# Kernel tuning notes

Hardware: AMD Instinct MI355X
Metric: run time of the kernel (lower is better)

Reference implementation:

```python
import jax, jax.numpy as jnp
import numpy as np

H = W = 128
SCALE = 4
Q = (SCALE * H) * (SCALE * W)
C = 64
E = 4


def _conv2d(x, w, b, pad):
    y = jax.lax.conv_general_dilated(x, w, (1, 1), [(pad, pad), (pad, pad)],
                                     dimension_numbers=('NCHW', 'OIHW', 'NCHW'))
    return y + b[None, :, None, None]


def _conv1x1(x, w, b):
    return jnp.einsum('oc,bchw->bohw', w, x) + b[None, :, None, None]


def _bilinear_zeros(img, gx, gy):
    # img: [C,Hs,Ws]; gx,gy: [Hh,Wh] normalized coords, align_corners=True, zeros padding
    c, Hs, Ws = img.shape
    x = (gx + 1.0) * 0.5 * (Ws - 1)
    y = (gy + 1.0) * 0.5 * (Hs - 1)
    x0 = jnp.floor(x)
    y0 = jnp.floor(y)
    wx1 = x - x0; wx0 = 1.0 - wx1
    wy1 = y - y0; wy0 = 1.0 - wy1
    x0i = x0.astype(jnp.int32); y0i = y0.astype(jnp.int32)

    def gather(yi, xi):
        m = ((xi >= 0) & (xi < Ws) & (yi >= 0) & (yi < Hs)).astype(img.dtype)
        v = img[:, jnp.clip(yi, 0, Hs - 1), jnp.clip(xi, 0, Ws - 1)]
        return v * m  # [C,Hh,Wh]

    return (gather(y0i, x0i) * (wy0 * wx0) + gather(y0i, x0i + 1) * (wy0 * wx1)
            + gather(y0i + 1, x0i) * (wy1 * wx0) + gather(y0i + 1, x0i + 1) * (wy1 * wx1))


def setup_inputs() -> dict:
    key = jax.random.key(0)
    ks = jax.random.split(key, 18)
    s = 0.1
    d = {}
    d['inp'] = jax.random.normal(ks[0], (1, 3, H, W), jnp.float32)
    d['coord'] = jax.random.uniform(ks[1], (1, Q, 2), jnp.float32, -1.0, 1.0)
    d['cell'] = jnp.full((1, Q, 2), 2.0 / (SCALE * H), jnp.float32)  # cell = 2/(scale*h) exactly
    d['enc_w'] = jax.random.normal(ks[2], (C, 3, 3, 3), jnp.float32) * s
    d['enc_b'] = jax.random.normal(ks[3], (C,), jnp.float32) * s
    d['body_w1'] = jax.random.normal(ks[4], (C, 4), jnp.float32) * s
    d['body_b1'] = jax.random.normal(ks[5], (C,), jnp.float32) * s
    d['body_w2'] = jax.random.normal(ks[6], (C, C), jnp.float32) * s
    d['body_b2'] = jax.random.normal(ks[7], (C,), jnp.float32) * s
    d['routing_w'] = jax.random.normal(ks[8], (E, C), jnp.float32) * s
    d['routing_b'] = jax.random.normal(ks[9], (E,), jnp.float32) * s
    d['offset_w'] = jax.random.normal(ks[10], (2, C), jnp.float32) * s
    d['offset_b'] = jax.random.normal(ks[11], (2,), jnp.float32) * s
    d['tail_w'] = jax.random.normal(ks[12], (3, C, 3, 3), jnp.float32) * s
    d['tail_b'] = jax.random.normal(ks[13], (3,), jnp.float32) * s
    d['weight_compress'] = jax.random.normal(ks[14], (E, C // 8, C), jnp.float32) * s
    d['weight_expand'] = jax.random.normal(ks[15], (E, C, C // 8), jnp.float32) * s
    d['scale'] = SCALE
    return d


def reference(inp, coord, cell, enc_w, enc_b, body_w1, body_b1, body_w2, body_b2,
              routing_w, routing_b, offset_w, offset_b, tail_w, tail_b,
              weight_compress, weight_expand, scale):
    feat = _conv2d(inp, enc_w, enc_b, pad=1)        # encoder -> [1,64,h,w]
    _, c, h, w = feat.shape
    Hh, Wh = scale * h, scale * w
    fs = float(scale)

    # scale embedding input: [1/scale, 1/scale, coor_h, coor_w]
    ih = jnp.arange(Hh, dtype=jnp.float32)
    iw = jnp.arange(Wh, dtype=jnp.float32)
    coor_h = (ih + 0.5) / fs - jnp.floor((ih + 0.5) / fs + 0.001) - 0.5
    coor_w = (iw + 0.5) / fs - jnp.floor((iw + 0.5) / fs + 0.001) - 0.5
    cs = jnp.full((Hh, Wh), 1.0 / fs, jnp.float32)
    inp4 = jnp.stack([cs, cs,
                      jnp.broadcast_to(coor_h[:, None], (Hh, Wh)),
                      jnp.broadcast_to(coor_w[None, :], (Hh, Wh))])[None]  # [1,4,Hh,Wh]

    emb = jax.nn.relu(_conv1x1(inp4, body_w1, body_b1))
    emb = jax.nn.relu(_conv1x1(emb, body_w2, body_b2))
    off = _conv1x1(emb, offset_w, offset_b)[0]                 # [2,Hh,Wh]
    r = jax.nn.sigmoid(_conv1x1(emb, routing_w, routing_b))[0]  # [E,Hh,Wh]

    # offset grid_sample of LR feat onto HR grid (align_corners=True, zeros pad)
    xx, yy = jnp.meshgrid(jnp.arange(Wh, dtype=jnp.float32), jnp.arange(Hh, dtype=jnp.float32))
    gx = (((xx + 0.5) / fs - 0.5) * 2.0 / (w - 1) - 1.0) + off[0] * 2.0 / (w - 1)
    gy = (((yy + 0.5) / fs - 0.5) * 2.0 / (h - 1) - 1.0) + off[1] * 2.0 / (h - 1)
    fea0 = _bilinear_zeros(feat[0], gx, gy)                    # [c,Hh,Wh]

    # per-pixel expert mixing; linear in routing, so apply experts then mix
    t = jnp.einsum('ekc,chw->ekhw', weight_compress, fea0)     # [E,c/8,Hh,Wh]
    mid = jnp.einsum('ehw,ekhw->khw', r, t)                    # [c/8,Hh,Wh]
    u = jnp.einsum('eck,khw->echw', weight_expand, mid)        # [E,c,Hh,Wh]
    out2 = jnp.einsum('ehw,echw->chw', r, u)                   # [c,Hh,Wh]

    pred = _conv2d((out2 + fea0)[None], tail_w, tail_b, pad=1)[0]  # [3,Hh,Wh]

    # nearest-neighbour query (align_corners=True)
    coord_q = jnp.clip(coord - cell * 0.5 + 1e-6, -1.0 + 1e-6, 1.0 - 1e-6)[0]  # [Q,2] (y,x)
    gxq = coord_q[:, 1]
    gyq = coord_q[:, 0]
    xi = jnp.clip(jnp.round((gxq + 1.0) * 0.5 * (Wh - 1)).astype(jnp.int32), 0, Wh - 1)
    yi = jnp.clip(jnp.round((gyq + 1.0) * 0.5 * (Hh - 1)).astype(jnp.int32), 0, Hh - 1)
    q = pred[:, yi, xi].T                                      # [Q,3]
    return q[None]                                             # [1,Q,3]
```

## Files before the change

kernel.cpp:

```cpp
#include <hip/hip_runtime.h>
#include <hip/hip_bf16.h>

typedef __hip_bfloat16 bf16;
typedef __fp16 h2 __attribute__((ext_vector_type(2)));

__device__ __forceinline__ float bf2f(bf16 h) { return __bfloat162float(h); }
__device__ __forceinline__ bf16 us2bf(unsigned short u){ union{unsigned short s; bf16 h;}v; v.s=u; return v.h; }
__device__ __forceinline__ float asf(unsigned u){ union{unsigned u; float f;}v; v.u=u; return v.f; }
__device__ __forceinline__ h2 uh(unsigned u){ union{unsigned u; h2 h;}v; v.u=u; return v.h; }
__device__ __forceinline__ unsigned pkh(float a, float b){ union{h2 h; unsigned u;}v; v.h=__builtin_amdgcn_cvt_pkrtz(a,b); return v.u; }
__device__ __forceinline__ unsigned short f2bu(float a){ union{bf16 h; unsigned short u;}v; v.h=__float2bfloat16(a); return v.u; }
__device__ __forceinline__ unsigned pkbf(float a, float b){ return ((unsigned)f2bu(b) << 16) | (unsigned)f2bu(a); }
#define FDOT2(va,vb,acc) __builtin_amdgcn_fdot2((va),(vb),(acc),false)

#define HH 128
#define WW 128
#define HS 512
#define WSZ 512
#define QN (HS*WSZ)

#define O_OFFTAB 0
#define O_TB     32
#define O_TW2    64
#define O_CWC2   1024
#define O_W2P    5120
#define O_FEAT   8192
#define O_PRED   1056768

#define SH_W2T 0
#define SH_WE  4160
#define SH_WC  6208
#define SH_TW  8256
#define SH_OW  9984
#define SH_RW  10112
#define SH_END 10368

__constant__ int PREF2[16] = {0,15,27,39,54,64,72,80,90,100,108,116,126,141,153,165};

__device__ __forceinline__ float rdin(const void* p, int i, bool f32m) {
  return f32m ? ((const float*)p)[i] : bf2f(((const bf16*)p)[i]);
}
__device__ __forceinline__ float rdw(const void* p, int i, bool f32m) {
  if (f32m) return ((const float*)p)[i];
  unsigned u = ((const unsigned*)p)[i>>1];
  return asf((i&1) ? (u & 0xffff0000u) : (u<<16));
}
__device__ __forceinline__ bool sniff_f32(const void* inp) {
  int lane = threadIdx.x & 63;
  unsigned short u = ((const unsigned short*)inp)[2*lane];
  float v = bf2f(us2bf(u));
  bool ok = (v == v) && (fabsf(v) < 64.0f);
  return __popcll(__ballot(ok)) < 48;
}
__device__ __forceinline__ unsigned blend4(unsigned a, unsigned b, unsigned c, unsigned d,
                                           h2 W00, h2 W01, h2 W10, h2 W11) {
  h2 f = uh(a)*W00 + uh(b)*W01 + uh(c)*W10 + uh(d)*W11;
  union{h2 h; unsigned u;} v; v.h = f; return v.u;
}

__global__ __launch_bounds__(256) void k_prep(
    const void* __restrict__ inp, const void* __restrict__ encw, const void* __restrict__ encb,
    const void* __restrict__ w1, const void* __restrict__ b1,
    const void* __restrict__ w2, const void* __restrict__ b2,
    const void* __restrict__ rw, const void* __restrict__ rb,
    const void* __restrict__ ow, const void* __restrict__ ob,
    const void* __restrict__ tw, const void* __restrict__ tb,
    const void* __restrict__ wc, const void* __restrict__ we,
    float* __restrict__ ws) {
  __shared__ float shpool[SH_END];
  __shared__ float sh1[64];
  __shared__ float sh2[64];
  __shared__ float shr[4];
  __shared__ float shcwe[512];
  bool f32m = sniff_f32(inp);
  int b = blockIdx.x, t = threadIdx.x;
  unsigned* wsu = (unsigned*)ws;

  if (b < 256) {
    int g = b >> 6;
    int px = (b & 63)*256 + t;
    float* shw = shpool;
    float* shb = shpool + 432;
    for (int i = t; i < 432; i += 256) shw[i] = rdw(encw, g*432 + i, f32m);
    if (t < 16) shb[t] = rdw(encb, g*16 + t, f32m);
    __syncthreads();
    int x = px & 127, y = px >> 7;
    float tp[27];
    #pragma unroll
    for (int ic = 0; ic < 3; ic++)
      #pragma unroll
      for (int dy = 0; dy < 3; dy++) {
        int yy = y + dy - 1;
        #pragma unroll
        for (int dx = 0; dx < 3; dx++) {
          int xx = x + dx - 1;
          bool ok = (yy >= 0) & (yy < 128) & (xx >= 0) & (xx < 128);
          tp[ic*9 + dy*3 + dx] = ok ? rdin(inp, ic*16384 + yy*128 + xx, f32m) : 0.0f;
        }
      }
    unsigned e[8];
    #pragma unroll
    for (int o4 = 0; o4 < 4; o4++) {
      float a[4];
      #pragma unroll
      for (int oo = 0; oo < 4; oo++) {
        int o2 = o4*4 + oo;
        float acc = shb[o2];
        #pragma unroll
        for (int kk = 0; kk < 27; kk++) acc = fmaf(shw[o2*27 + kk], tp[kk], acc);
        a[oo] = acc;
      }
      e[o4*2]   = pkh(a[0], a[1]);
      e[o4*2+1] = pkh(a[2], a[3]);
    }
    uint4* outp = (uint4*)(wsu + O_FEAT + px*32 + g*8);
    outp[0] = make_uint4(e[0], e[1], e[2], e[3]);
    outp[1] = make_uint4(e[4], e[5], e[6], e[7]);
  } else if (b < 272) {
    int cls = b - 256;
    for (int i = t; i < 4096; i += 256) shpool[SH_W2T + (i & 63)*65 + (i >> 6)] = rdw(w2, i, f32m);
    for (int i = t; i < 2048; i += 256) { shpool[SH_WE + i] = rdw(we, i, f32m); shpool[SH_WC + i] = rdw(wc, i, f32m); }
    for (int i = t; i < 1728; i += 256) shpool[SH_TW + i] = rdw(tw, i, f32m);
    for (int i = t; i < 128; i += 256)  shpool[SH_OW + i] = rdw(ow, i, f32m);
    for (int i = t; i < 256; i += 256)  shpool[SH_RW + i] = rdw(rw, i, f32m);
    if (t < 64) {
      float mcls = (float)(cls >> 2), ncls = (float)(cls & 3);
      float chv = (mcls + 0.5f)*0.25f - 0.5f;
      float cwv = (ncls + 0.5f)*0.25f - 0.5f;
      float s1 = rdw(w1,t*4+0,f32m)*0.25f + rdw(w1,t*4+1,f32m)*0.25f
               + rdw(w1,t*4+2,f32m)*chv + rdw(w1,t*4+3,f32m)*cwv + rdw(b1,t,f32m);
      sh1[t] = fmaxf(s1, 0.0f);
    }
    __syncthreads();
    if (t < 64) {
      float s2 = rdw(b2,t,f32m);
      for (int i = 0; i < 64; i++) s2 = fmaf(shpool[SH_W2T + i*65 + t], sh1[i], s2);
      sh2[t] = fmaxf(s2, 0.0f);
    }
    __syncthreads();
    if (t < 2) {
      float a = rdw(ob,t,f32m);
      for (int i = 0; i < 64; i++) a = fmaf(shpool[SH_OW + t*64 + i], sh2[i], a);
      ws[O_OFFTAB + cls*2 + t] = a;
    } else if (t < 6) {
      int e = t - 2;
      float a = rdw(rb,e,f32m);
      for (int i = 0; i < 64; i++) a = fmaf(shpool[SH_RW + e*64 + i], sh2[i], a);
      shr[e] = 1.0f / (1.0f + expf(-a));
    }
    __syncthreads();
    float r0 = shr[0], r1 = shr[1], r2 = shr[2], r3 = shr[3];
    for (int idx = t; idx < 512; idx += 256) {
      float a =       r0 * shpool[SH_WE + idx];
      a = fmaf(r1, shpool[SH_WE +  512 + idx], a);
      a = fmaf(r2, shpool[SH_WE + 1024 + idx], a);
      a = fmaf(r3, shpool[SH_WE + 1536 + idx], a);
      shcwe[idx] = a;
    }
    unsigned* wcw = wsu + O_CWC2 + cls*256;
    for (int idx = t; idx < 256; idx += 256) {
      int cp = idx >> 3, k = idx & 7;
      float lo =       r0 * shpool[SH_WC +        k*64 + 2*cp];
      lo = fmaf(r1, shpool[SH_WC +  512 + k*64 + 2*cp], lo);
      lo = fmaf(r2, shpool[SH_WC + 1024 + k*64 + 2*cp], lo);
      lo = fmaf(r3, shpool[SH_WC + 1536 + k*64 + 2*cp], lo);
      float hi =       r0 * shpool[SH_WC +        k*64 + 2*cp + 1];
      hi = fmaf(r1, shpool[SH_WC +  512 + k*64 + 2*cp + 1], hi);
      hi = fmaf(r2, shpool[SH_WC + 1024 + k*64 + 2*cp + 1], hi);
      hi = fmaf(r3, shpool[SH_WC + 1536 + k*64 + 2*cp + 1], hi);
      wcw[idx] = pkh(lo, hi);
    }
    __syncthreads();
    unsigned* wpp = wsu + O_W2P;
    for (int idx = t; idx < 108; idx += 256) {
      int j = idx / 12, rem = idx - j*12, o2 = rem >> 2, kp = rem & 3;
      float alo = 0.0f, ahi = 0.0f;
      for (int c = 0; c < 64; c++) {
        float tv = shpool[SH_TW + (o2*64 + c)*9 + j];
        alo = fmaf(tv, shcwe[c*8 + 2*kp],     alo);
        ahi = fmaf(tv, shcwe[c*8 + 2*kp + 1], ahi);
      }
      wpp[(cls*9 + j)*12 + o2*4 + kp] = pkh(alo, ahi);
    }
  } else {
    for (int idx = t; idx < 864; idx += 256) {
      int o2 = idx / 288, rem = idx - o2*288, j = rem >> 5, cp = rem & 31;
      unsigned d = pkh(rdw(tw, (o2*64 + 2*cp    )*9 + j, f32m),
                       rdw(tw, (o2*64 + 2*cp + 1)*9 + j, f32m));
      (wsu + O_TW2)[idx] = d;
    }
    if (t < 3) ws[O_TB + t] = rdin(tb, t, f32m);
  }
}

__global__ __launch_bounds__(256) void k_maintail(const float* __restrict__ ws, unsigned* __restrict__ pred4) {
  __shared__ unsigned shf[32*181];
  __shared__ __align__(16) unsigned shm4[181*4];
  __shared__ unsigned short sof[192];
  __shared__ unsigned short scls[192];
  __shared__ float spart[128*3];
  const unsigned* wsu = (const unsigned*)ws;
  int blk = blockIdx.x;
  int xcd = blk & 7, local = blk >> 3;
  int ty0 = (xcd*8 + (local >> 5)) * 8;
  int tx0 = (local & 31) * 16;
  int t = threadIdx.x;
  int q = t & 1;
  const uint4* F2 = (const uint4*)(wsu + O_FEAT);

  for (int s0 = 0; s0 < 256; s0 += 128) {
    int s = s0 + (t >> 1);
    if (s >= 180) continue;
    int cls = 0;
    #pragma unroll
    for (int i = 1; i < 16; i++) cls += (s >= PREF2[i]) ? 1 : 0;
    int j = s - PREF2[cls];
    int a = cls >> 2, bb = cls & 3;
    int nx = ((bb == 0) | (bb == 3)) ? 5 : 4;
    int jy = (nx == 4) ? (j >> 2) : ((j*13) >> 6);
    int jx = j - jy*nx;
    int py = ((a + 1) & 3) + 4*jy;
    int px = ((bb + 1) & 3) + 4*jx;
    int pos = py*18 + px;
    if (q == 0) sof[pos] = (unsigned short)s;
    int gy = ty0 - 1 + py, gx = tx0 - 1 + px;
    if ((gy < 0) | (gy >= HS) | (gx < 0) | (gx >= WSZ)) {
      if (q == 0) scls[s] = 0;
      #pragma unroll
      for (int i = 0; i < 16; i++) shf[(q*16 + i)*181 + s] = 0u;
      shm4[s*4 + q*2 + 0] = 0u;
      shm4[s*4 + q*2 + 1] = 0u;
      continue;
    }
    if (q == 0) scls[s] = (unsigned short)cls;
    float off0 = ws[O_OFFTAB + cls*2 + 0];
    float off1 = ws[O_OFFTAB + cls*2 + 1];
    float gxf = (((float)gx + 0.5f)*0.25f - 0.5f)*(2.0f/127.0f) - 1.0f + off0*(2.0f/127.0f);
    float gyf = (((float)gy + 0.5f)*0.25f - 0.5f)*(2.0f/127.0f) - 1.0f + off1*(2.0f/127.0f);
    float sx = (gxf + 1.0f)*0.5f*127.0f;
    float sy = (gyf + 1.0f)*0.5f*127.0f;
    float x0f = floorf(sx), y0f = floorf(sy);
    float fx = sx - x0f, fy = sy - y0f;
    int ix0 = (int)x0f, iy0 = (int)y0f;
    int ix1 = ix0 + 1, iy1 = iy0 + 1;
    float wx0 = 1.0f - fx, wy0 = 1.0f - fy;
    float w00 = wy0*wx0, w01 = wy0*fx, w10 = fy*wx0, w11 = fy*fx;
    bool vx0 = (ix0 >= 0) & (ix0 < WW), vx1 = (ix1 >= 0) & (ix1 < WW);
    bool vy0 = (iy0 >= 0) & (iy0 < HH), vy1 = (iy1 >= 0) & (iy1 < HH);
    if (!(vy0 & vx0)) w00 = 0.0f;
    if (!(vy0 & vx1)) w01 = 0.0f;
    if (!(vy1 & vx0)) w10 = 0.0f;
    if (!(vy1 & vx1)) w11 = 0.0f;
    int cx0 = min(max(ix0, 0), WW-1), cx1 = min(max(ix1, 0), WW-1);
    int cy0 = min(max(iy0, 0), HH-1), cy1 = min(max(iy1, 0), HH-1);
    int b00 = (cy0*WW + cx0)*8 + q*4, b01 = (cy0*WW + cx1)*8 + q*4;
    int b10 = (cy1*WW + cx0)*8 + q*4, b11 = (cy1*WW + cx1)*8 + q*4;

    uint4 A0 = F2[b00+0], A1 = F2[b00+1], A2 = F2[b00+2], A3 = F2[b00+3];
    uint4 B0 = F2[b01+0], B1 = F2[b01+1], B2 = F2[b01+2], B3 = F2[b01+3];
    uint4 C0 = F2[b10+0], C1 = F2[b10+1], C2 = F2[b10+2], C3 = F2[b10+3];
    uint4 D0 = F2[b11+0], D1 = F2[b11+1], D2 = F2[b11+2], D3 = F2[b11+3];

    h2 W00 = { (__fp16)w00, (__fp16)w00 };
    h2 W01 = { (__fp16)w01, (__fp16)w01 };
    h2 W10 = { (__fp16)w10, (__fp16)w10 };
    h2 W11 = { (__fp16)w11, (__fp16)w11 };

    unsigned fp[16];
    fp[ 0] = blend4(A0.x,B0.x,C0.x,D0.x,W00,W01,W10,W11);
    fp[ 1] = blend4(A0.y,B0.y,C0.y,D0.y,W00,W01,W10,W11);
    fp[ 2] = blend4(A0.z,B0.z,C0.z,D0.z,W00,W01,W10,W11);
    fp[ 3] = blend4(A0.w,B0.w,C0.w,D0.w,W00,W01,W10,W11);
    fp[ 4] = blend4(A1.x,B1.x,C1.x,D1.x,W00,W01,W10,W11);
    fp[ 5] = blend4(A1.y,B1.y,C1.y,D1.y,W00,W01,W10,W11);
    fp[ 6] = blend4(A1.z,B1.z,C1.z,D1.z,W00,W01,W10,W11);
    fp[ 7] = blend4(A1.w,B1.w,C1.w,D1.w,W00,W01,W10,W11);
    fp[ 8] = blend4(A2.x,B2.x,C2.x,D2.x,W00,W01,W10,W11);
    fp[ 9] = blend4(A2.y,B2.y,C2.y,D2.y,W00,W01,W10,W11);
    fp[10] = blend4(A2.z,B2.z,C2.z,D2.z,W00,W01,W10,W11);
    fp[11] = blend4(A2.w,B2.w,C2.w,D2.w,W00,W01,W10,W11);
    fp[12] = blend4(A3.x,B3.x,C3.x,D3.x,W00,W01,W10,W11);
    fp[13] = blend4(A3.y,B3.y,C3.y,D3.y,W00,W01,W10,W11);
    fp[14] = blend4(A3.z,B3.z,C3.z,D3.z,W00,W01,W10,W11);
    fp[15] = blend4(A3.w,B3.w,C3.w,D3.w,W00,W01,W10,W11);

    #pragma unroll
    for (int i = 0; i < 16; i++) shf[(q*16 + i)*181 + s] = fp[i];

    const uint4* CWv = (const uint4*)(wsu + O_CWC2 + cls*256) + q*32;
    float mid[8] = {0,0,0,0,0,0,0,0};
    #pragma unroll
    for (int i = 0; i < 16; i++) {
      uint4 w0 = CWv[i*2], w1 = CWv[i*2+1];
      h2 f = uh(fp[i]);
      mid[0] = FDOT2(f, uh(w0.x), mid[0]); mid[1] = FDOT2(f, uh(w0.y), mid[1]);
      mid[2] = FDOT2(f, uh(w0.z), mid[2]); mid[3] = FDOT2(f, uh(w0.w), mid[3]);
      mid[4] = FDOT2(f, uh(w1.x), mid[4]); mid[5] = FDOT2(f, uh(w1.y), mid[5]);
      mid[6] = FDOT2(f, uh(w1.z), mid[6]); mid[7] = FDOT2(f, uh(w1.w), mid[7]);
    }
    #pragma unroll
    for (int k = 0; k < 8; k++) mid[k] += __shfl_xor(mid[k], 1);
    shm4[s*4 + q*2 + 0] = pkh(mid[q*4+0], mid[q*4+1]);
    shm4[s*4 + q*2 + 1] = pkh(mid[q*4+2], mid[q*4+3]);
  }
  __syncthreads();

  int half = t >> 7, pi = t & 127;
  int tx = pi & 15, ty = pi >> 4;
  int slots[9];
  #pragma unroll
  for (int dy = 0; dy < 3; dy++)
    #pragma unroll
    for (int dx = 0; dx < 3; dx++)
      slots[dy*3 + dx] = sof[(ty + dy)*18 + (tx + dx)];
  const unsigned* TW2 = wsu + O_TW2;
  float a0, a1, a2;
  if (half == 0) { a0 = ws[O_TB+0]; a1 = ws[O_TB+1]; a2 = ws[O_TB+2]; }
  else           { a0 = 0.0f; a1 = 0.0f; a2 = 0.0f; }
  int cp0 = half*16;
  for (int cpl = 0; cpl < 16; cpl++) {
    int cp = cp0 + cpl;
    #pragma unroll
    for (int j = 0; j < 9; j++) {
      h2 hv = uh(shf[cp*181 + slots[j]]);
      a0 = FDOT2(hv, uh(TW2[(0*9 + j)*32 + cp]), a0);
      a1 = FDOT2(hv, uh(TW2[(1*9 + j)*32 + cp]), a1);
      a2 = FDOT2(hv, uh(TW2[(2*9 + j)*32 + cp]), a2);
    }
  }
  {
    int jb = (half == 0) ? 0 : 5;
    int je = (half == 0) ? 5 : 9;
    for (int j = jb; j < je; j++) {
      int sl = slots[j];
      int cl = scls[sl];
      uint4 mv = *(const uint4*)&shm4[sl*4];
      const uint4* Wp = (const uint4*)(wsu + O_W2P) + (cl*9 + j)*3;
      uint4 w0 = Wp[0], w1 = Wp[1], w2 = Wp[2];
      h2 m0 = uh(mv.x), m1 = uh(mv.y), m2 = uh(mv.z), m3 = uh(mv.w);
      a0 = FDOT2(m0, uh(w0.x), a0); a0 = FDOT2(m1, uh(w0.y), a0);
      a0 = FDOT2(m2, uh(w0.z), a0); a0 = FDOT2(m3, uh(w0.w), a0);
      a1 = FDOT2(m0, uh(w1.x), a1); a1 = FDOT2(m1, uh(w1.y), a1);
      a1 = FDOT2(m2, uh(w1.z), a1); a1 = FDOT2(m3, uh(w1.w), a1);
      a2 = FDOT2(m0, uh(w2.x), a2); a2 = FDOT2(m1, uh(w2.y), a2);
      a2 = FDOT2(m2, uh(w2.z), a2); a2 = FDOT2(m3, uh(w2.w), a2);
    }
  }
  if (half == 1) {
    spart[pi*3+0] = a0; spart[pi*3+1] = a1; spart[pi*3+2] = a2;
  }
  __syncthreads();
  if (half == 0) {
    a0 += spart[pi*3+0]; a1 += spart[pi*3+1]; a2 += spart[pi*3+2];
    ((uint2*)pred4)[blk*128 + pi] = make_uint2(pkbf(a0, a1), pkbf(a2, 0.0f));
  }
}

__global__ __launch_bounds__(256) void k_gather(const void* __restrict__ inp,
                                                const void* __restrict__ coord, const void* __restrict__ cell,
                                                const float* __restrict__ ws, void* __restrict__ outp) {
  bool f32m = sniff_f32(inp);
  const uint2* pred4 = (const uint2*)((const unsigned*)ws + O_PRED);
  int q = blockIdx.x*256 + threadIdx.x;
  float cy, cx, ly, lx;
  if (f32m) {
    float2 c = ((const float2*)coord)[q]; cy = c.x; cx = c.y;
    float2 l = ((const float2*)cell)[q];  ly = l.x; lx = l.y;
  } else {
    unsigned cu = ((const unsigned*)coord)[q]; cy = asf(cu<<16); cx = asf(cu & 0xffff0000u);
    unsigned lu = ((const unsigned*)cell)[q];  ly = asf(lu<<16); lx = asf(lu & 0xffff0000u);
  }
  float gyq = fminf(fmaxf(cy - ly*0.5f + 1e-6f, -1.0f + 1e-6f), 1.0f - 1e-6f);
  float gxq = fminf(fmaxf(cx - lx*0.5f + 1e-6f, -1.0f + 1e-6f), 1.0f - 1e-6f);
  int xi = (int)rintf((gxq + 1.0f)*0.5f*511.0f);
  int yi = (int)rintf((gyq + 1.0f)*0.5f*511.0f);
  xi = min(max(xi, 0), WSZ-1);
  yi = min(max(yi, 0), HS-1);
  int row = yi >> 3, col = xi >> 4;
  int xcd = row >> 3;
  int local = (row & 7)*32 + col;
  int blk = local*8 + xcd;
  int pi = (yi & 7)*16 + (xi & 15);
  uint2 d = pred4[blk*128 + pi];
  float v0 = asf(d.x << 16), v1 = asf(d.x & 0xffff0000u), v2 = asf(d.y << 16);
  if (f32m) {
    float* o = (float*)outp;
    o[q*3 + 0] = v0; o[q*3 + 1] = v1; o[q*3 + 2] = v2;
  } else {
    bf16* o = (bf16*)outp;
    o[q*3 + 0] = __float2bfloat16(v0);
    o[q*3 + 1] = __float2bfloat16(v1);
    o[q*3 + 2] = __float2bfloat16(v2);
  }
}

extern "C" void kernel_launch(void* const* d_in, const int* in_sizes, int n_in,
                              void* d_out, int out_size, void* d_ws, size_t ws_size,
                              hipStream_t stream) {
  const void* inp   = d_in[0];
  const void* coord = d_in[1];
  const void* cell  = d_in[2];
  const void* encw  = d_in[3];
  const void* encb  = d_in[4];
  const void* w1    = d_in[5];
  const void* b1    = d_in[6];
  const void* w2    = d_in[7];
  const void* b2    = d_in[8];
  const void* rw    = d_in[9];
  const void* rb    = d_in[10];
  const void* ow    = d_in[11];
  const void* ob    = d_in[12];
  const void* tw    = d_in[13];
  const void* tb    = d_in[14];
  const void* wc    = d_in[15];
  const void* we    = d_in[16];

  float* wsf = (float*)d_ws;
  unsigned* pred4 = (unsigned*)wsf + O_PRED;

  k_prep<<<273, 256, 0, stream>>>(inp, encw, encb, w1, b1, w2, b2, rw, rb, ow, ob, tw, tb, wc, we, wsf);
  k_maintail<<<2048, 256, 0, stream>>>(wsf, pred4);
  k_gather<<<1024, 256, 0, stream>>>(inp, coord, cell, wsf, d_out);
}
```

Before: 176.8 us.

## Double block size in main tail kernel, split conv into four partial sums

```diff
diff --git a/kernel.cpp b/kernel.cpp
--- a/kernel.cpp
+++ b/kernel.cpp
@@ -193,12 +193,11 @@
   }
 }
 
-__global__ __launch_bounds__(256) void k_maintail(const float* __restrict__ ws, unsigned* __restrict__ pred4) {
+__global__ __launch_bounds__(512) void k_maintail(const float* __restrict__ ws, unsigned* __restrict__ pred4) {
   __shared__ unsigned shf[32*181];
   __shared__ __align__(16) unsigned shm4[181*4];
-  __shared__ unsigned short sof[192];
   __shared__ unsigned short scls[192];
-  __shared__ float spart[128*3];
+  __shared__ float spart[3*384];
   const unsigned* wsu = (const unsigned*)ws;
   int blk = blockIdx.x;
   int xcd = blk & 7, local = blk >> 3;
@@ -208,9 +207,8 @@
   int q = t & 1;
   const uint4* F2 = (const uint4*)(wsu + O_FEAT);
 
-  for (int s0 = 0; s0 < 256; s0 += 128) {
-    int s = s0 + (t >> 1);
-    if (s >= 180) continue;
+  int s = t >> 1;
+  if (s < 180) {
     int cls = 0;
     #pragma unroll
     for (int i = 1; i < 16; i++) cls += (s >= PREF2[i]) ? 1 : 0;
@@ -222,119 +220,119 @@
     int py = ((a + 1) & 3) + 4*jy;
     int px = ((bb + 1) & 3) + 4*jx;
     int pos = py*18 + px;
-    if (q == 0) sof[pos] = (unsigned short)s;
     int gy = ty0 - 1 + py, gx = tx0 - 1 + px;
     if ((gy < 0) | (gy >= HS) | (gx < 0) | (gx >= WSZ)) {
-      if (q == 0) scls[s] = 0;
-      #pragma unroll
-      for (int i = 0; i < 16; i++) shf[(q*16 + i)*181 + s] = 0u;
-      shm4[s*4 + q*2 + 0] = 0u;
-      shm4[s*4 + q*2 + 1] = 0u;
-      continue;
-    }
-    if (q == 0) scls[s] = (unsigned short)cls;
-    float off0 = ws[O_OFFTAB + cls*2 + 0];
-    float off1 = ws[O_OFFTAB + cls*2 + 1];
-    float gxf = (((float)gx + 0.5f)*0.25f - 0.5f)*(2.0f/127.0f) - 1.0f + off0*(2.0f/127.0f);
-    float gyf = (((float)gy + 0.5f)*0.25f - 0.5f)*(2.0f/127.0f) - 1.0f + off1*(2.0f/127.0f);
-    float sx = (gxf + 1.0f)*0.5f*127.0f;
-    float sy = (gyf + 1.0f)*0.5f*127.0f;
-    float x0f = floorf(sx), y0f = floorf(sy);
-    float fx = sx - x0f, fy = sy - y0f;
-    int ix0 = (int)x0f, iy0 = (int)y0f;
-    int ix1 = ix0 + 1, iy1 = iy0 + 1;
-    float wx0 = 1.0f - fx, wy0 = 1.0f - fy;
-    float w00 = wy0*wx0, w01 = wy0*fx, w10 = fy*wx0, w11 = fy*fx;
-    bool vx0 = (ix0 >= 0) & (ix0 < WW), vx1 = (ix1 >= 0) & (ix1 < WW);
-    bool vy0 = (iy0 >= 0) & (iy0 < HH), vy1 = (iy1 >= 0) & (iy1 < HH);
-    if (!(vy0 & vx0)) w00 = 0.0f;
-    if (!(vy0 & vx1)) w01 = 0.0f;
-    if (!(vy1 & vx0)) w10 = 0.0f;
-    if (!(vy1 & vx1)) w11 = 0.0f;
-    int cx0 = min(max(ix0, 0), WW-1), cx1 = min(max(ix1, 0), WW-1);
-    int cy0 = min(max(iy0, 0), HH-1), cy1 = min(max(iy1, 0), HH-1);
-    int b00 = (cy0*WW + cx0)*8 + q*4, b01 = (cy0*WW + cx1)*8 + q*4;
-    int b10 = (cy1*WW + cx0)*8 + q*4, b11 = (cy1*WW + cx1)*8 + q*4;
-
-    uint4 A0 = F2[b00+0], A1 = F2[b00+1], A2 = F2[b00+2], A3 = F2[b00+3];
-    uint4 B0 = F2[b01+0], B1 = F2[b01+1], B2 = F2[b01+2], B3 = F2[b01+3];
-    uint4 C0 = F2[b10+0], C1 = F2[b10+1], C2 = F2[b10+2], C3 = F2[b10+3];
-    uint4 D0 = F2[b11+0], D1 = F2[b11+1], D2 = F2[b11+2], D3 = F2[b11+3];
-
-    h2 W00 = { (__fp16)w00, (__fp16)w00 };
-    h2 W01 = { (__fp16)w01, (__fp16)w01 };
-    h2 W10 = { (__fp16)w10, (__fp16)w10 };
-    h2 W11 = { (__fp16)w11, (__fp16)w11 };
-
-    unsigned fp[16];
-    fp[ 0] = blend4(A0.x,B0.x,C0.x,D0.x,W00,W01,W10,W11);
-    fp[ 1] = blend4(A0.y,B0.y,C0.y,D0.y,W00,W01,W10,W11);
-    fp[ 2] = blend4(A0.z,B0.z,C0.z,D0.z,W00,W01,W10,W11);
-    fp[ 3] = blend4(A0.w,B0.w,C0.w,D0.w,W00,W01,W10,W11);
-    fp[ 4] = blend4(A1.x,B1.x,C1.x,D1.x,W00,W01,W10,W11);
-    fp[ 5] = blend4(A1.y,B1.y,C1.y,D1.y,W00,W01,W10,W11);
-    fp[ 6] = blend4(A1.z,B1.z,C1.z,D1.z,W00,W01,W10,W11);
-    fp[ 7] = blend4(A1.w,B1.w,C1.w,D1.w,W00,W01,W10,W11);
-    fp[ 8] = blend4(A2.x,B2.x,C2.x,D2.x,W00,W01,W10,W11);
-    fp[ 9] = blend4(A2.y,B2.y,C2.y,D2.y,W00,W01,W10,W11);
-    fp[10] = blend4(A2.z,B2.z,C2.z,D2.z,W00,W01,W10,W11);
-    fp[11] = blend4(A2.w,B2.w,C2.w,D2.w,W00,W01,W10,W11);
-    fp[12] = blend4(A3.x,B3.x,C3.x,D3.x,W00,W01,W10,W11);
-    fp[13] = blend4(A3.y,B3.y,C3.y,D3.y,W00,W01,W10,W11);
-    fp[14] = blend4(A3.z,B3.z,C3.z,D3.z,W00,W01,W10,W11);
-    fp[15] = blend4(A3.w,B3.w,C3.w,D3.w,W00,W01,W10,W11);
-
-    #pragma unroll
-    for (int i = 0; i < 16; i++) shf[(q*16 + i)*181 + s] = fp[i];
-
-    const uint4* CWv = (const uint4*)(wsu + O_CWC2 + cls*256) + q*32;
-    float mid[8] = {0,0,0,0,0,0,0,0};
-    #pragma unroll
-    for (int i = 0; i < 16; i++) {
-      uint4 w0 = CWv[i*2], w1 = CWv[i*2+1];
-      h2 f = uh(fp[i]);
-      mid[0] = FDOT2(f, uh(w0.x), mid[0]); mid[1] = FDOT2(f, uh(w0.y), mid[1]);
-      mid[2] = FDOT2(f, uh(w0.z), mid[2]); mid[3] = FDOT2(f, uh(w0.w), mid[3]);
-      mid[4] = FDOT2(f, uh(w1.x), mid[4]); mid[5] = FDOT2(f, uh(w1.y), mid[5]);
-      mid[6] = FDOT2(f, uh(w1.z), mid[6]); mid[7] = FDOT2(f, uh(w1.w), mid[7]);
-    }
-    #pragma unroll
-    for (int k = 0; k < 8; k++) mid[k] += __shfl_xor(mid[k], 1);
-    shm4[s*4 + q*2 + 0] = pkh(mid[q*4+0], mid[q*4+1]);
-    shm4[s*4 + q*2 + 1] = pkh(mid[q*4+2], mid[q*4+3]);
+      if (q == 0) scls[pos] = 0;
+      #pragma unroll
+      for (int i = 0; i < 16; i++) shf[(q*16 + i)*181 + pos] = 0u;
+      shm4[pos*4 + q*2 + 0] = 0u;
+      shm4[pos*4 + q*2 + 1] = 0u;
+    } else {
+      if (q == 0) scls[pos] = (unsigned short)cls;
+      float off0 = ws[O_OFFTAB + cls*2 + 0];
+      float off1 = ws[O_OFFTAB + cls*2 + 1];
+      float gxf = (((float)gx + 0.5f)*0.25f - 0.5f)*(2.0f/127.0f) - 1.0f + off0*(2.0f/127.0f);
+      float gyf = (((float)gy + 0.5f)*0.25f - 0.5f)*(2.0f/127.0f) - 1.0f + off1*(2.0f/127.0f);
+      float sx = (gxf + 1.0f)*0.5f*127.0f;
+      float sy = (gyf + 1.0f)*0.5f*127.0f;
+      float x0f = floorf(sx), y0f = floorf(sy);
+      float fx = sx - x0f, fy = sy - y0f;
+      int ix0 = (int)x0f, iy0 = (int)y0f;
+      int ix1 = ix0 + 1, iy1 = iy0 + 1;
+      float wx0 = 1.0f - fx, wy0 = 1.0f - fy;
+      float w00 = wy0*wx0, w01 = wy0*fx, w10 = fy*wx0, w11 = fy*fx;
+      bool vx0 = (ix0 >= 0) & (ix0 < WW), vx1 = (ix1 >= 0) & (ix1 < WW);
+      bool vy0 = (iy0 >= 0) & (iy0 < HH), vy1 = (iy1 >= 0) & (iy1 < HH);
+      if (!(vy0 & vx0)) w00 = 0.0f;
+      if (!(vy0 & vx1)) w01 = 0.0f;
+      if (!(vy1 & vx0)) w10 = 0.0f;
+      if (!(vy1 & vx1)) w11 = 0.0f;
+      int cx0 = min(max(ix0, 0), WW-1), cx1 = min(max(ix1, 0), WW-1);
+      int cy0 = min(max(iy0, 0), HH-1), cy1 = min(max(iy1, 0), HH-1);
+      int b00 = (cy0*WW + cx0)*8 + q*4, b01 = (cy0*WW + cx1)*8 + q*4;
+      int b10 = (cy1*WW + cx0)*8 + q*4, b11 = (cy1*WW + cx1)*8 + q*4;
+
+      uint4 A0 = F2[b00+0], A1 = F2[b00+1], A2 = F2[b00+2], A3 = F2[b00+3];
+      uint4 B0 = F2[b01+0], B1 = F2[b01+1], B2 = F2[b01+2], B3 = F2[b01+3];
+      uint4 C0 = F2[b10+0], C1 = F2[b10+1], C2 = F2[b10+2], C3 = F2[b10+3];
+      uint4 D0 = F2[b11+0], D1 = F2[b11+1], D2 = F2[b11+2], D3 = F2[b11+3];
+
+      h2 W00 = { (__fp16)w00, (__fp16)w00 };
+      h2 W01 = { (__fp16)w01, (__fp16)w01 };
+      h2 W10 = { (__fp16)w10, (__fp16)w10 };
+      h2 W11 = { (__fp16)w11, (__fp16)w11 };
+
+      unsigned fp[16];
+      fp[ 0] = blend4(A0.x,B0.x,C0.x,D0.x,W00,W01,W10,W11);
+      fp[ 1] = blend4(A0.y,B0.y,C0.y,D0.y,W00,W01,W10,W11);
+      fp[ 2] = blend4(A0.z,B0.z,C0.z,D0.z,W00,W01,W10,W11);
+      fp[ 3] = blend4(A0.w,B0.w,C0.w,D0.w,W00,W01,W10,W11);
+      fp[ 4] = blend4(A1.x,B1.x,C1.x,D1.x,W00,W01,W10,W11);
+      fp[ 5] = blend4(A1.y,B1.y,C1.y,D1.y,W00,W01,W10,W11);
+      fp[ 6] = blend4(A1.z,B1.z,C1.z,D1.z,W00,W01,W10,W11);
+      fp[ 7] = blend4(A1.w,B1.w,C1.w,D1.w,W00,W01,W10,W11);
+      fp[ 8] = blend4(A2.x,B2.x,C2.x,D2.x,W00,W01,W10,W11);
+      fp[ 9] = blend4(A2.y,B2.y,C2.y,D2.y,W00,W01,W10,W11);
+      fp[10] = blend4(A2.z,B2.z,C2.z,D2.z,W00,W01,W10,W11);
+      fp[11] = blend4(A2.w,B2.w,C2.w,D2.w,W00,W01,W10,W11);
+      fp[12] = blend4(A3.x,B3.x,C3.x,D3.x,W00,W01,W10,W11);
+      fp[13] = blend4(A3.y,B3.y,C3.y,D3.y,W00,W01,W10,W11);
+      fp[14] = blend4(A3.z,B3.z,C3.z,D3.z,W00,W01,W10,W11);
+      fp[15] = blend4(A3.w,B3.w,C3.w,D3.w,W00,W01,W10,W11);
+
+      #pragma unroll
+      for (int i = 0; i < 16; i++) shf[(q*16 + i)*181 + pos] = fp[i];
+
+      const uint4* CWv = (const uint4*)(wsu + O_CWC2 + cls*256) + q*32;
+      float mid[8] = {0,0,0,0,0,0,0,0};
+      #pragma unroll
+      for (int i = 0; i < 16; i++) {
+        uint4 w0 = CWv[i*2], w1 = CWv[i*2+1];
+        h2 f = uh(fp[i]);
+        mid[0] = FDOT2(f, uh(w0.x), mid[0]); mid[1] = FDOT2(f, uh(w0.y), mid[1]);
+        mid[2] = FDOT2(f, uh(w0.z), mid[2]); mid[3] = FDOT2(f, uh(w0.w), mid[3]);
+        mid[4] = FDOT2(f, uh(w1.x), mid[4]); mid[5] = FDOT2(f, uh(w1.y), mid[5]);
+        mid[6] = FDOT2(f, uh(w1.z), mid[6]); mid[7] = FDOT2(f, uh(w1.w), mid[7]);
+      }
+      #pragma unroll
+      for (int k = 0; k < 8; k++) mid[k] += __shfl_xor(mid[k], 1);
+      shm4[pos*4 + q*2 + 0] = pkh(mid[q*4+0], mid[q*4+1]);
+      shm4[pos*4 + q*2 + 1] = pkh(mid[q*4+2], mid[q*4+3]);
+    }
   }
   __syncthreads();
 
-  int half = t >> 7, pi = t & 127;
+  int split = t >> 7, pi = t & 127;
   int tx = pi & 15, ty = pi >> 4;
-  int slots[9];
+  int pos9[9];
   #pragma unroll
   for (int dy = 0; dy < 3; dy++)
     #pragma unroll
     for (int dx = 0; dx < 3; dx++)
-      slots[dy*3 + dx] = sof[(ty + dy)*18 + (tx + dx)];
+      pos9[dy*3 + dx] = (ty + dy)*18 + (tx + dx);
   const unsigned* TW2 = wsu + O_TW2;
   float a0, a1, a2;
-  if (half == 0) { a0 = ws[O_TB+0]; a1 = ws[O_TB+1]; a2 = ws[O_TB+2]; }
-  else           { a0 = 0.0f; a1 = 0.0f; a2 = 0.0f; }
-  int cp0 = half*16;
-  for (int cpl = 0; cpl < 16; cpl++) {
+  if (split == 0) { a0 = ws[O_TB+0]; a1 = ws[O_TB+1]; a2 = ws[O_TB+2]; }
+  else            { a0 = 0.0f; a1 = 0.0f; a2 = 0.0f; }
+  int cp0 = split*8;
+  for (int cpl = 0; cpl < 8; cpl++) {
     int cp = cp0 + cpl;
     #pragma unroll
     for (int j = 0; j < 9; j++) {
-      h2 hv = uh(shf[cp*181 + slots[j]]);
+      h2 hv = uh(shf[cp*181 + pos9[j]]);
       a0 = FDOT2(hv, uh(TW2[(0*9 + j)*32 + cp]), a0);
       a1 = FDOT2(hv, uh(TW2[(1*9 + j)*32 + cp]), a1);
       a2 = FDOT2(hv, uh(TW2[(2*9 + j)*32 + cp]), a2);
     }
   }
   {
-    int jb = (half == 0) ? 0 : 5;
-    int je = (half == 0) ? 5 : 9;
+    const int JB[4] = {0, 2, 5, 7};
+    const int JE[4] = {2, 5, 7, 9};
+    int jb = JB[split], je = JE[split];
     for (int j = jb; j < je; j++) {
-      int sl = slots[j];
-      int cl = scls[sl];
-      uint4 mv = *(const uint4*)&shm4[sl*4];
+      int pp = pos9[j];
+      int cl = scls[pp];
+      uint4 mv = *(const uint4*)&shm4[pp*4];
       const uint4* Wp = (const uint4*)(wsu + O_W2P) + (cl*9 + j)*3;
       uint4 w0 = Wp[0], w1 = Wp[1], w2 = Wp[2];
       h2 m0 = uh(mv.x), m1 = uh(mv.y), m2 = uh(mv.z), m3 = uh(mv.w);
@@ -346,12 +344,17 @@
       a2 = FDOT2(m2, uh(w2.z), a2); a2 = FDOT2(m3, uh(w2.w), a2);
     }
   }
-  if (half == 1) {
-    spart[pi*3+0] = a0; spart[pi*3+1] = a1; spart[pi*3+2] = a2;
+  if (split != 0) {
+    float* sp = spart + (split-1)*384 + pi*3;
+    sp[0] = a0; sp[1] = a1; sp[2] = a2;
   }
   __syncthreads();
-  if (half == 0) {
-    a0 += spart[pi*3+0]; a1 += spart[pi*3+1]; a2 += spart[pi*3+2];
+  if (split == 0) {
+    #pragma unroll
+    for (int k = 0; k < 3; k++) {
+      const float* sp = spart + k*384 + pi*3;
+      a0 += sp[0]; a1 += sp[1]; a2 += sp[2];
+    }
     ((uint2*)pred4)[blk*128 + pi] = make_uint2(pkbf(a0, a1), pkbf(a2, 0.0f));
   }
 }
@@ -419,6 +422,6 @@
   unsigned* pred4 = (unsigned*)wsf + O_PRED;
 
   k_prep<<<273, 256, 0, stream>>>(inp, encw, encb, w1, b1, w2, b2, rw, rb, ow, ob, tw, tb, wc, we, wsf);
-  k_maintail<<<2048, 256, 0, stream>>>(wsf, pred4);
+  k_maintail<<<2048, 512, 0, stream>>>(wsf, pred4);
   k_gather<<<1024, 256, 0, stream>>>(inp, coord, cell, wsf, d_out);
 }
```

After: 181.5 us. +2.7%, slower.

## Store tile features pixel-major in LDS with vectorized reads and staged compress weights

Applied to the files above, without the earlier changes.

```diff
diff --git a/kernel.cpp b/kernel.cpp
--- a/kernel.cpp
+++ b/kernel.cpp
@@ -17,7 +17,6 @@
 #define WW 128
 #define HS 512
 #define WSZ 512
-#define QN (HS*WSZ)
 
 #define O_OFFTAB 0
 #define O_TB     32
@@ -194,10 +193,9 @@
 }
 
 __global__ __launch_bounds__(256) void k_maintail(const float* __restrict__ ws, unsigned* __restrict__ pred4) {
-  __shared__ unsigned shf[32*181];
-  __shared__ __align__(16) unsigned shm4[181*4];
-  __shared__ unsigned short sof[192];
-  __shared__ unsigned short scls[192];
+  __shared__ __align__(16) unsigned shd[180*36];
+  __shared__ __align__(16) unsigned shcw[32*132];
+  __shared__ unsigned short scls[180];
   __shared__ float spart[128*3];
   const unsigned* wsu = (const unsigned*)ws;
   int blk = blockIdx.x;
@@ -208,6 +206,17 @@
   int q = t & 1;
   const uint4* F2 = (const uint4*)(wsu + O_FEAT);
 
+  {
+    const uint4* src = (const uint4*)(wsu + O_CWC2);
+    #pragma unroll
+    for (int k = 0; k < 4; k++) {
+      int e = t + k*256;
+      int combo = e >> 5, idx = e & 31;
+      ((uint4*)&shcw[combo*132])[idx] = src[e];
+    }
+  }
+  __syncthreads();
+
   for (int s0 = 0; s0 < 256; s0 += 128) {
     int s = s0 + (t >> 1);
     if (s >= 180) continue;
@@ -222,17 +231,19 @@
     int py = ((a + 1) & 3) + 4*jy;
     int px = ((bb + 1) & 3) + 4*jx;
     int pos = py*18 + px;
-    if (q == 0) sof[pos] = (unsigned short)s;
+    unsigned* row = &shd[pos*36 + q*16];
     int gy = ty0 - 1 + py, gx = tx0 - 1 + px;
     if ((gy < 0) | (gy >= HS) | (gx < 0) | (gx >= WSZ)) {
-      if (q == 0) scls[s] = 0;
-      #pragma unroll
-      for (int i = 0; i < 16; i++) shf[(q*16 + i)*181 + s] = 0u;
-      shm4[s*4 + q*2 + 0] = 0u;
-      shm4[s*4 + q*2 + 1] = 0u;
+      if (q == 0) scls[pos] = 0;
+      ((uint4*)row)[0] = make_uint4(0,0,0,0);
+      ((uint4*)row)[1] = make_uint4(0,0,0,0);
+      ((uint4*)row)[2] = make_uint4(0,0,0,0);
+      ((uint4*)row)[3] = make_uint4(0,0,0,0);
+      shd[pos*36 + 32 + q*2 + 0] = 0u;
+      shd[pos*36 + 32 + q*2 + 1] = 0u;
       continue;
     }
-    if (q == 0) scls[s] = (unsigned short)cls;
+    if (q == 0) scls[pos] = (unsigned short)cls;
     float off0 = ws[O_OFFTAB + cls*2 + 0];
     float off1 = ws[O_OFFTAB + cls*2 + 1];
     float gxf = (((float)gx + 0.5f)*0.25f - 0.5f)*(2.0f/127.0f) - 1.0f + off0*(2.0f/127.0f);
@@ -284,10 +295,12 @@
     fp[14] = blend4(A3.z,B3.z,C3.z,D3.z,W00,W01,W10,W11);
     fp[15] = blend4(A3.w,B3.w,C3.w,D3.w,W00,W01,W10,W11);
 
-    #pragma unroll
-    for (int i = 0; i < 16; i++) shf[(q*16 + i)*181 + s] = fp[i];
-
-    const uint4* CWv = (const uint4*)(wsu + O_CWC2 + cls*256) + q*32;
+    ((uint4*)row)[0] = make_uint4(fp[0],  fp[1],  fp[2],  fp[3]);
+    ((uint4*)row)[1] = make_uint4(fp[4],  fp[5],  fp[6],  fp[7]);
+    ((uint4*)row)[2] = make_uint4(fp[8],  fp[9],  fp[10], fp[11]);
+    ((uint4*)row)[3] = make_uint4(fp[12], fp[13], fp[14], fp[15]);
+
+    const uint4* CWv = (const uint4*)&shcw[(cls*2 + q)*132];
     float mid[8] = {0,0,0,0,0,0,0,0};
     #pragma unroll
     for (int i = 0; i < 16; i++) {
@@ -300,41 +313,43 @@
     }
     #pragma unroll
     for (int k = 0; k < 8; k++) mid[k] += __shfl_xor(mid[k], 1);
-    shm4[s*4 + q*2 + 0] = pkh(mid[q*4+0], mid[q*4+1]);
-    shm4[s*4 + q*2 + 1] = pkh(mid[q*4+2], mid[q*4+3]);
+    shd[pos*36 + 32 + q*2 + 0] = pkh(mid[q*4+0], mid[q*4+1]);
+    shd[pos*36 + 32 + q*2 + 1] = pkh(mid[q*4+2], mid[q*4+3]);
   }
   __syncthreads();
 
   int half = t >> 7, pi = t & 127;
   int tx = pi & 15, ty = pi >> 4;
-  int slots[9];
-  #pragma unroll
-  for (int dy = 0; dy < 3; dy++)
-    #pragma unroll
-    for (int dx = 0; dx < 3; dx++)
-      slots[dy*3 + dx] = sof[(ty + dy)*18 + (tx + dx)];
   const unsigned* TW2 = wsu + O_TW2;
   float a0, a1, a2;
   if (half == 0) { a0 = ws[O_TB+0]; a1 = ws[O_TB+1]; a2 = ws[O_TB+2]; }
   else           { a0 = 0.0f; a1 = 0.0f; a2 = 0.0f; }
-  int cp0 = half*16;
-  for (int cpl = 0; cpl < 16; cpl++) {
-    int cp = cp0 + cpl;
-    #pragma unroll
-    for (int j = 0; j < 9; j++) {
-      h2 hv = uh(shf[cp*181 + slots[j]]);
-      a0 = FDOT2(hv, uh(TW2[(0*9 + j)*32 + cp]), a0);
-      a1 = FDOT2(hv, uh(TW2[(1*9 + j)*32 + cp]), a1);
-      a2 = FDOT2(hv, uh(TW2[(2*9 + j)*32 + cp]), a2);
-    }
-  }
-  {
-    int jb = (half == 0) ? 0 : 5;
-    int je = (half == 0) ? 5 : 9;
-    for (int j = jb; j < je; j++) {
-      int sl = slots[j];
-      int cl = scls[sl];
-      uint4 mv = *(const uint4*)&shm4[sl*4];
+  int cb = half*16;
+  #pragma unroll
+  for (int j = 0; j < 9; j++) {
+    int dy = j / 3, dx = j - dy*3;
+    int pp = (ty + dy)*18 + (tx + dx);
+    const uint4* frow = (const uint4*)&shd[pp*36 + half*16];
+    uint4 f0 = frow[0], f1 = frow[1], f2 = frow[2], f3 = frow[3];
+    const unsigned* T0 = TW2 + (0*9+j)*32 + cb;
+    const unsigned* T1 = TW2 + (1*9+j)*32 + cb;
+    const unsigned* T2 = TW2 + (2*9+j)*32 + cb;
+    a0=FDOT2(uh(f0.x),uh(T0[0]),a0); a0=FDOT2(uh(f0.y),uh(T0[1]),a0); a0=FDOT2(uh(f0.z),uh(T0[2]),a0); a0=FDOT2(uh(f0.w),uh(T0[3]),a0);
+    a0=FDOT2(uh(f1.x),uh(T0[4]),a0); a0=FDOT2(uh(f1.y),uh(T0[5]),a0); a0=FDOT2(uh(f1.z),uh(T0[6]),a0); a0=FDOT2(uh(f1.w),uh(T0[7]),a0);
+    a0=FDOT2(uh(f2.x),uh(T0[8]),a0); a0=FDOT2(uh(f2.y),uh(T0[9]),a0); a0=FDOT2(uh(f2.z),uh(T0[10]),a0); a0=FDOT2(uh(f2.w),uh(T0[11]),a0);
+    a0=FDOT2(uh(f3.x),uh(T0[12]),a0); a0=FDOT2(uh(f3.y),uh(T0[13]),a0); a0=FDOT2(uh(f3.z),uh(T0[14]),a0); a0=FDOT2(uh(f3.w),uh(T0[15]),a0);
+    a1=FDOT2(uh(f0.x),uh(T1[0]),a1); a1=FDOT2(uh(f0.y),uh(T1[1]),a1); a1=FDOT2(uh(f0.z),uh(T1[2]),a1); a1=FDOT2(uh(f0.w),uh(T1[3]),a1);
+    a1=FDOT2(uh(f1.x),uh(T1[4]),a1); a1=FDOT2(uh(f1.y),uh(T1[5]),a1); a1=FDOT2(uh(f1.z),uh(T1[6]),a1); a1=FDOT2(uh(f1.w),uh(T1[7]),a1);
+    a1=FDOT2(uh(f2.x),uh(T1[8]),a1); a1=FDOT2(uh(f2.y),uh(T1[9]),a1); a1=FDOT2(uh(f2.z),uh(T1[10]),a1); a1=FDOT2(uh(f2.w),uh(T1[11]),a1);
+    a1=FDOT2(uh(f3.x),uh(T1[12]),a1); a1=FDOT2(uh(f3.y),uh(T1[13]),a1); a1=FDOT2(uh(f3.z),uh(T1[14]),a1); a1=FDOT2(uh(f3.w),uh(T1[15]),a1);
+    a2=FDOT2(uh(f0.x),uh(T2[0]),a2); a2=FDOT2(uh(f0.y),uh(T2[1]),a2); a2=FDOT2(uh(f0.z),uh(T2[2]),a2); a2=FDOT2(uh(f0.w),uh(T2[3]),a2);
+    a2=FDOT2(uh(f1.x),uh(T2[4]),a2); a2=FDOT2(uh(f1.y),uh(T2[5]),a2); a2=FDOT2(uh(f1.z),uh(T2[6]),a2); a2=FDOT2(uh(f1.w),uh(T2[7]),a2);
+    a2=FDOT2(uh(f2.x),uh(T2[8]),a2); a2=FDOT2(uh(f2.y),uh(T2[9]),a2); a2=FDOT2(uh(f2.z),uh(T2[10]),a2); a2=FDOT2(uh(f2.w),uh(T2[11]),a2);
+    a2=FDOT2(uh(f3.x),uh(T2[12]),a2); a2=FDOT2(uh(f3.y),uh(T2[13]),a2); a2=FDOT2(uh(f3.z),uh(T2[14]),a2); a2=FDOT2(uh(f3.w),uh(T2[15]),a2);
+    bool mine = (half == 0) ? (j < 5) : (j >= 5);
+    if (mine) {
+      int cl = scls[pp];
+      uint4 mv = *(const uint4*)&shd[pp*36 + 32];
       const uint4* Wp = (const uint4*)(wsu + O_W2P) + (cl*9 + j)*3;
       uint4 w0 = Wp[0], w1 = Wp[1], w2 = Wp[2];
       h2 m0 = uh(mv.x), m1 = uh(mv.y), m2 = uh(mv.z), m3 = uh(mv.w);
```

Result: faster. 160.1 us (-9.5%).
